# Optimization experiments

Measured on AMD Instinct MI355X. Metric: run time of the kernel, lower is better.

Reference implementation:

```python
import jax, jax.numpy as jnp
import numpy as np

B, T, D, H = 512, 256, 256, 1024


def setup_inputs() -> dict:
    key = jax.random.key(0)
    ks = jax.random.split(key, 8)
    s = 1.0 / np.sqrt(3 * D)
    return {
        "X": jax.random.normal(ks[0], (B, T, D), dtype=jnp.float32),
        "M": (jax.random.uniform(ks[1], (B, T, D)) < 0.5).astype(jnp.float32),
        "input_means": jax.random.normal(ks[2], (D,), dtype=jnp.float32) * 0.1,
        "gamma_x": jnp.ones((D,), dtype=jnp.float32),
        "Wz": jax.random.normal(ks[3], (H, 3 * D), dtype=jnp.float32) * s,
        "bz": jnp.zeros((H,), dtype=jnp.float32),
        "Wr": jax.random.normal(ks[4], (H, 3 * D), dtype=jnp.float32) * s,
        "br": jnp.zeros((H,), dtype=jnp.float32),
        "Wh": jax.random.normal(ks[5], (H, 3 * D), dtype=jnp.float32) * s,
        "bh": jnp.zeros((H,), dtype=jnp.float32),
        "Wout": jax.random.normal(ks[6], (1, H), dtype=jnp.float32) * (1.0 / np.sqrt(H)),
        "bout": jnp.zeros((1,), dtype=jnp.float32),
    }


def reference(X, M, input_means, gamma_x, Wz, bz, Wr, br, Wh, bh, Wout, bout):
    Bc, Tc, Dc = X.shape
    xm = input_means  # [D], broadcast as the per-timestep mean
    xm_b = jnp.broadcast_to(xm, (Bc, Dc))

    def step(h, xt_mt):
        x_t, m_t = xt_mt  # each [B, D]
        x_hat = m_t * x_t + (1.0 - m_t) * xm
        g = jnp.exp(-gamma_x * (1.0 - m_t))  # input decay
        x_tilde = g * x_hat + (1.0 - g) * xm
        inp = jnp.concatenate([x_tilde, xm_b, m_t], axis=1)  # [B, 3D]
        z_t = jax.nn.sigmoid(inp @ Wz.T + bz)
        r_t = jax.nn.sigmoid(inp @ Wr.T + br)  # computed but unused (faithful to source)
        h_til = jnp.tanh(inp @ Wh.T + bh)
        h_new = (1.0 - z_t) * h + z_t * h_til
        return h_new, None

    h0 = jnp.zeros((Bc, Wz.shape[0]), dtype=X.dtype)
    # scan over time: only the final hidden state feeds the output head
    h_last, _ = jax.lax.scan(step, h0, (jnp.swapaxes(X, 0, 1), jnp.swapaxes(M, 0, 1)))
    out = jax.nn.sigmoid(h_last @ Wout.T + bout)  # [B, 1]
    return out.squeeze(1)  # [B]
```

## Files before the change

### kernel.cpp

```cpp
#include <hip/hip_runtime.h>
#include <cstdint>
#include <cstddef>

#define B_  512
#define T_  256
#define D_  256
#define H_  1024
#define K2  512
#define N2  2048
#define TC  32
#define NCHUNK 8

#define OFF_WB    ((size_t)0)
#define OFF_CVEC  ((size_t)2097152)
#define OFF_H     ((size_t)2105344)
#define OFF_PQ    ((size_t)4202496)
#define OFF_INP2  ((size_t)37756928)
#define WS_BIG    ((size_t)171974656)

typedef short   bf16x8 __attribute__((ext_vector_type(8)));
typedef float   f32x4  __attribute__((ext_vector_type(4)));

__device__ __forceinline__ unsigned short f2bf(float f) {
    unsigned int u = __float_as_uint(f);
    u += 0x7fffu + ((u >> 16) & 1u);
    return (unsigned short)(u >> 16);
}
__device__ __forceinline__ float bf2f(unsigned short s) {
    return __uint_as_float(((unsigned int)s) << 16);
}
__device__ __forceinline__ void async16(const void* g, void* l) {
    __builtin_amdgcn_global_load_lds(
        (const __attribute__((address_space(1))) void*)g,
        (__attribute__((address_space(3))) void*)l, 16, 0, 0);
}

__global__ void build_wb(const float* __restrict__ Wz, const float* __restrict__ Wh,
                         const float* __restrict__ xm, unsigned short* __restrict__ Wb) {
    int e = blockIdx.x * 256 + threadIdx.x;
    int r = e >> 9;
    int k = e & 511;
    int m = r >> 1;
    const float* W = (r & 1) ? (Wh + (size_t)m * 768) : (Wz + (size_t)m * 768);
    float v = (k < D_) ? W[k]
                       : (W[2 * D_ + (k - D_)] - W[k - D_] * xm[k - D_]);
    Wb[e] = f2bf(v);
}

__global__ void build_cvec(const float* __restrict__ Wz, const float* __restrict__ bz,
                           const float* __restrict__ Wh, const float* __restrict__ bh,
                           const float* __restrict__ xm, float* __restrict__ cvec) {
    int r = blockIdx.x;
    int m = r >> 1;
    int d = threadIdx.x;
    const float* W = (r & 1) ? (Wh + (size_t)m * 768) : (Wz + (size_t)m * 768);
    float v = (W[d] + W[D_ + d]) * xm[d];
    for (int off = 32; off; off >>= 1) v += __shfl_down(v, off);
    __shared__ float red[4];
    if ((d & 63) == 0) red[d >> 6] = v;
    __syncthreads();
    if (d == 0) {
        float bias = (r & 1) ? bh[m] : bz[m];
        cvec[r] = bias + red[0] + red[1] + red[2] + red[3];
    }
}

__global__ void build_inp2(const float* __restrict__ X, const float* __restrict__ Mm,
                           unsigned short* __restrict__ inp2, int chunk0) {
    int g = blockIdx.x * 256 + threadIdx.x;
    int r = g >> 6;
    int k = (g & 63) * 8;
    int c  = chunk0 + (r >> 14);
    int rl = r & 16383;
    int b  = rl >> 5;
    int tc = rl & 31;
    int t  = c * TC + tc;
    int d  = (k < D_) ? k : (k - D_);
    const float4* mp = (const float4*)(Mm + ((size_t)b * T_ + t) * D_ + d);
    float4 m0 = mp[0], m1 = mp[1];
    unsigned short o[8];
    if (k < D_) {
        const float4* xp = (const float4*)(X + ((size_t)b * T_ + t) * D_ + d);
        float4 x0 = xp[0], x1 = xp[1];
        o[0]=f2bf(m0.x*x0.x); o[1]=f2bf(m0.y*x0.y); o[2]=f2bf(m0.z*x0.z); o[3]=f2bf(m0.w*x0.w);
        o[4]=f2bf(m1.x*x1.x); o[5]=f2bf(m1.y*x1.y); o[6]=f2bf(m1.z*x1.z); o[7]=f2bf(m1.w*x1.w);
    } else {
        o[0]=f2bf(m0.x); o[1]=f2bf(m0.y); o[2]=f2bf(m0.z); o[3]=f2bf(m0.w);
        o[4]=f2bf(m1.x); o[5]=f2bf(m1.y); o[6]=f2bf(m1.z); o[7]=f2bf(m1.w);
    }
    uint4 pk;
    pk.x = (unsigned)o[0] | ((unsigned)o[1] << 16);
    pk.y = (unsigned)o[2] | ((unsigned)o[3] << 16);
    pk.z = (unsigned)o[4] | ((unsigned)o[5] << 16);
    pk.w = (unsigned)o[6] | ((unsigned)o[7] << 16);
    *(uint4*)(inp2 + (size_t)r * K2 + k) = pk;
}

#define EPAD 140
__global__ __launch_bounds__(256) void gemm_scan(
    const unsigned short* __restrict__ A,
    const unsigned short* __restrict__ W,
    const float* __restrict__ cvec,
    float2* __restrict__ PQ,
    int chunk0)
{
    __shared__ __align__(16) unsigned short sm[128 * EPAD];
    const int tid  = threadIdx.x;
    const int lane = tid & 63;
    const int w    = tid >> 6;
    const int tn = blockIdx.x, tmg = blockIdx.y;
    const int wm = w & 1, wn = w >> 1;

    const int seg  = w * 2;
    const int srow = seg * 16 + (lane >> 2);
    const int scol = (lane & 3) * 8;
    const int aoff = seg * 512;
    const unsigned short* aptr = A + (size_t)(tmg * 128 + srow) * K2 + scol;
    const unsigned short* bptr = W + (size_t)(tn * 128 + srow) * K2 + scol;

#define STAGE(nxt, k0)                                              \
    { unsigned short* ad = sm + (nxt) * 4096 + aoff;                \
      unsigned short* bd = sm + 8192 + (nxt) * 4096 + aoff;         \
      async16(aptr + (k0),            ad);                          \
      async16(aptr + 16 * K2 + (k0),  ad + 512);                    \
      async16(bptr + (k0),            bd);                          \
      async16(bptr + 16 * K2 + (k0),  bd + 512); }

    f32x4 acc[4][4] = {};

    STAGE(0, 0);
    __syncthreads();

    for (int t = 0; t < 16; ++t) {
        const int cur = t & 1;
        if (t < 15) STAGE(cur ^ 1, (t + 1) * 32);
        const unsigned short* Ab = sm + cur * 4096;
        const unsigned short* Bb = sm + 8192 + cur * 4096;
        bf16x8 af[4], bv[4];
        #pragma unroll
        for (int i = 0; i < 4; i++)
            af[i] = *(const bf16x8*)&Ab[(wm*64 + i*16 + (lane & 15)) * 32 + (lane >> 4) * 8];
        #pragma unroll
        for (int j = 0; j < 4; j++)
            bv[j] = *(const bf16x8*)&Bb[(wn*64 + j*16 + (lane & 15)) * 32 + (lane >> 4) * 8];
        #pragma unroll
        for (int i = 0; i < 4; i++)
            #pragma unroll
            for (int j = 0; j < 4; j++)
                acc[i][j] = __builtin_amdgcn_mfma_f32_16x16x32_bf16(af[i], bv[j], acc[i][j], 0, 0, 0);
        __syncthreads();
    }
#undef STAGE

    const float p = (float)(lane & 1);
    const float sg = 1.f + p;
    #pragma unroll
    for (int j = 0; j < 4; j++) {
        const int ncol  = tn*128 + wn*64 + j*16 + (lane & 15);
        const int col_l = wn*64 + j*16 + (lane & 15);
        const float cadd = cvec[ncol];
        #pragma unroll
        for (int i = 0; i < 4; i++) {
            const int rbase = wm*64 + i*16 + (lane >> 4) * 4;
            #pragma unroll
            for (int r = 0; r < 4; r++) {
                float v = acc[i][j][r] + cadd;
                float u = __expf(-sg * v);
                float res = sg / (1.f + u) - p;
                sm[(size_t)(rbase + r) * EPAD + col_l] = f2bf(res);
            }
        }
    }
    __syncthreads();

    const int bl = tid >> 6;
    const int np = tid & 63;
    const unsigned int* lds32 = (const unsigned int*)sm;
    float Pp = 1.f, Qq = 0.f;
    #pragma unroll
    for (int tc = 0; tc < 32; ++tc) {
        unsigned int zw = lds32[(size_t)(bl * 32 + tc) * (EPAD / 2) + np];
        float z  = bf2f((unsigned short)(zw & 0xffff));
        float ht = bf2f((unsigned short)(zw >> 16));
        float om = 1.f - z;
        Qq = om * Qq + z * ht;
        Pp = om * Pp;
    }
    const int c   = chunk0 + (tmg >> 7);
    const int bg  = (tmg & 127) * 4 + bl;
    const int npg = tn * 64 + np;
    PQ[((size_t)c * B_ + bg) * H_ + npg] = make_float2(Pp, Qq);
}

__global__ void combine(const float2* __restrict__ PQ, float* __restrict__ hbuf) {
    int v = blockIdx.x * 256 + threadIdx.x;
    int b = v >> 10;
    int n = v & 1023;
    float h = 0.f;
    #pragma unroll
    for (int c = 0; c < NCHUNK; c++) {
        float2 pq = PQ[((size_t)c * B_ + b) * H_ + n];
        h = pq.x * h + pq.y;
    }
    hbuf[(size_t)b * H_ + n] = h;
}

__global__ void head(const float* __restrict__ hbuf, const float* __restrict__ Wout,
                     const float* __restrict__ bout, float* __restrict__ out) {
    int b = blockIdx.x;
    float s = 0.f;
    for (int n = threadIdx.x; n < H_; n += 256)
        s += hbuf[(size_t)b * H_ + n] * Wout[n];
    for (int off = 32; off; off >>= 1) s += __shfl_down(s, off);
    __shared__ float red[4];
    if ((threadIdx.x & 63) == 0) red[threadIdx.x >> 6] = s;
    __syncthreads();
    if (threadIdx.x == 0) {
        float t = red[0] + red[1] + red[2] + red[3] + bout[0];
        out[b] = 1.f / (1.f + expf(-t));
    }
}

extern "C" void kernel_launch(void* const* d_in, const int* in_sizes, int n_in,
                              void* d_out, int out_size, void* d_ws, size_t ws_size,
                              hipStream_t stream) {
    const float* X    = (const float*)d_in[0];
    const float* Mm   = (const float*)d_in[1];
    const float* xm   = (const float*)d_in[2];
    const float* Wz   = (const float*)d_in[4];
    const float* bz   = (const float*)d_in[5];
    const float* Wh   = (const float*)d_in[8];
    const float* bh   = (const float*)d_in[9];
    const float* Wout = (const float*)d_in[10];
    const float* bout = (const float*)d_in[11];
    float* out = (float*)d_out;

    char* ws = (char*)d_ws;
    unsigned short* Wb    = (unsigned short*)(ws + OFF_WB);
    float*          cvec  = (float*)(ws + OFF_CVEC);
    float*          hbuf  = (float*)(ws + OFF_H);
    float2*         PQ    = (float2*)(ws + OFF_PQ);
    unsigned short* inp2  = (unsigned short*)(ws + OFF_INP2);

    build_wb  <<<dim3(N2 * K2 / 256), dim3(256), 0, stream>>>(Wz, Wh, xm, Wb);
    build_cvec<<<dim3(N2),            dim3(256), 0, stream>>>(Wz, bz, Wh, bh, xm, cvec);

    if (ws_size >= WS_BIG) {
        build_inp2<<<dim3(NCHUNK * TC * B_ * 64 / 256), dim3(256), 0, stream>>>(X, Mm, inp2, 0);
        gemm_scan <<<dim3(16, NCHUNK * TC * B_ / 128),  dim3(256), 0, stream>>>(inp2, Wb, cvec, PQ, 0);
    } else {
        for (int c = 0; c < NCHUNK; c++) {
            build_inp2<<<dim3(TC * B_ * 64 / 256), dim3(256), 0, stream>>>(X, Mm, inp2, c);
            gemm_scan <<<dim3(16, TC * B_ / 128),  dim3(256), 0, stream>>>(inp2, Wb, cvec, PQ, c);
        }
    }

    combine<<<dim3(B_ * H_ / 256), dim3(256), 0, stream>>>(PQ, hbuf);
    head   <<<dim3(B_),            dim3(256), 0, stream>>>(hbuf, Wout, bout, out);
}
```

Measured before the change: 714.4 us.

## Fuse input packing into GEMM-scan, keep full A tile in LDS, scan in registers

Drops the separate build_inp2 pass and its bf16 intermediate buffer. Each 512-thread block now converts its 128 rows of X*M and M to bf16 directly into LDS once, then sweeps all 2048 output columns, reading weights straight from global memory (L2) with no LDS staging. The per-chunk scan is done in registers using lane shuffles and an associative combine of (P,Q) pairs, replacing the LDS round-trip of activations. This removes a large global write and read of the packed input, but weight traffic now goes through L2 without sharing across waves, and the larger accumulator arrays increase register pressure.

Result: slower. 1.571 ms (+119.9%).

```diff
diff --git a/kernel.cpp b/kernel.cpp
--- a/kernel.cpp
+++ b/kernel.cpp
@@ -15,8 +15,6 @@
 #define OFF_CVEC  ((size_t)2097152)
 #define OFF_H     ((size_t)2105344)
 #define OFF_PQ    ((size_t)4202496)
-#define OFF_INP2  ((size_t)37756928)
-#define WS_BIG    ((size_t)171974656)
 
 typedef short   bf16x8 __attribute__((ext_vector_type(8)));
 typedef float   f32x4  __attribute__((ext_vector_type(4)));
@@ -25,14 +23,6 @@
     unsigned int u = __float_as_uint(f);
     u += 0x7fffu + ((u >> 16) & 1u);
     return (unsigned short)(u >> 16);
-}
-__device__ __forceinline__ float bf2f(unsigned short s) {
-    return __uint_as_float(((unsigned int)s) << 16);
-}
-__device__ __forceinline__ void async16(const void* g, void* l) {
-    __builtin_amdgcn_global_load_lds(
-        (const __attribute__((address_space(1))) void*)g,
-        (__attribute__((address_space(3))) void*)l, 16, 0, 0);
 }
 
 __global__ void build_wb(const float* __restrict__ Wz, const float* __restrict__ Wh,
@@ -65,131 +55,133 @@
     }
 }
 
-__global__ void build_inp2(const float* __restrict__ X, const float* __restrict__ Mm,
-                           unsigned short* __restrict__ inp2, int chunk0) {
-    int g = blockIdx.x * 256 + threadIdx.x;
-    int r = g >> 6;
-    int k = (g & 63) * 8;
-    int c  = chunk0 + (r >> 14);
-    int rl = r & 16383;
-    int b  = rl >> 5;
-    int tc = rl & 31;
-    int t  = c * TC + tc;
-    int d  = (k < D_) ? k : (k - D_);
-    const float4* mp = (const float4*)(Mm + ((size_t)b * T_ + t) * D_ + d);
-    float4 m0 = mp[0], m1 = mp[1];
-    unsigned short o[8];
-    if (k < D_) {
-        const float4* xp = (const float4*)(X + ((size_t)b * T_ + t) * D_ + d);
-        float4 x0 = xp[0], x1 = xp[1];
-        o[0]=f2bf(m0.x*x0.x); o[1]=f2bf(m0.y*x0.y); o[2]=f2bf(m0.z*x0.z); o[3]=f2bf(m0.w*x0.w);
-        o[4]=f2bf(m1.x*x1.x); o[5]=f2bf(m1.y*x1.y); o[6]=f2bf(m1.z*x1.z); o[7]=f2bf(m1.w*x1.w);
-    } else {
-        o[0]=f2bf(m0.x); o[1]=f2bf(m0.y); o[2]=f2bf(m0.z); o[3]=f2bf(m0.w);
-        o[4]=f2bf(m1.x); o[5]=f2bf(m1.y); o[6]=f2bf(m1.z); o[7]=f2bf(m1.w);
-    }
-    uint4 pk;
-    pk.x = (unsigned)o[0] | ((unsigned)o[1] << 16);
-    pk.y = (unsigned)o[2] | ((unsigned)o[3] << 16);
-    pk.z = (unsigned)o[4] | ((unsigned)o[5] << 16);
-    pk.w = (unsigned)o[6] | ((unsigned)o[7] << 16);
-    *(uint4*)(inp2 + (size_t)r * K2 + k) = pk;
-}
-
-#define EPAD 140
-__global__ __launch_bounds__(256) void gemm_scan(
-    const unsigned short* __restrict__ A,
+#define ASTRIDE 520
+__global__ __launch_bounds__(512, 2) void gemm_scan(
+    const float* __restrict__ X,
+    const float* __restrict__ Mm,
     const unsigned short* __restrict__ W,
     const float* __restrict__ cvec,
-    float2* __restrict__ PQ,
-    int chunk0)
+    float2* __restrict__ PQ)
 {
-    __shared__ __align__(16) unsigned short sm[128 * EPAD];
+    __shared__ __align__(16) unsigned short As[128 * ASTRIDE];
     const int tid  = threadIdx.x;
     const int lane = tid & 63;
     const int w    = tid >> 6;
-    const int tn = blockIdx.x, tmg = blockIdx.y;
-    const int wm = w & 1, wn = w >> 1;
-
-    const int seg  = w * 2;
-    const int srow = seg * 16 + (lane >> 2);
-    const int scol = (lane & 3) * 8;
-    const int aoff = seg * 512;
-    const unsigned short* aptr = A + (size_t)(tmg * 128 + srow) * K2 + scol;
-    const unsigned short* bptr = W + (size_t)(tn * 128 + srow) * K2 + scol;
-
-#define STAGE(nxt, k0)                                              \
-    { unsigned short* ad = sm + (nxt) * 4096 + aoff;                \
-      unsigned short* bd = sm + 8192 + (nxt) * 4096 + aoff;         \
-      async16(aptr + (k0),            ad);                          \
-      async16(aptr + 16 * K2 + (k0),  ad + 512);                    \
-      async16(bptr + (k0),            bd);                          \
-      async16(bptr + 16 * K2 + (k0),  bd + 512); }
-
-    f32x4 acc[4][4] = {};
-
-    STAGE(0, 0);
+    const int p    = blockIdx.x;
+    const int c    = p >> 7;
+    const int bg0  = (p & 127) * 4;
+
+    {
+        const int half = lane >> 5;
+        const int d    = (lane & 31) * 8;
+        #pragma unroll
+        for (int j = 0; j < 16; ++j) {
+            const int row = w + 8 * j;
+            const int b   = bg0 + (row >> 5);
+            const int t   = c * TC + (row & 31);
+            const size_t base = ((size_t)b * T_ + t) * D_ + d;
+            const float4* mp = (const float4*)(Mm + base);
+            float4 m0 = mp[0], m1 = mp[1];
+            float v[8];
+            if (half == 0) {
+                const float4* xp = (const float4*)(X + base);
+                float4 x0 = xp[0], x1 = xp[1];
+                v[0]=m0.x*x0.x; v[1]=m0.y*x0.y; v[2]=m0.z*x0.z; v[3]=m0.w*x0.w;
+                v[4]=m1.x*x1.x; v[5]=m1.y*x1.y; v[6]=m1.z*x1.z; v[7]=m1.w*x1.w;
+            } else {
+                v[0]=m0.x; v[1]=m0.y; v[2]=m0.z; v[3]=m0.w;
+                v[4]=m1.x; v[5]=m1.y; v[6]=m1.z; v[7]=m1.w;
+            }
+            uint4 pk;
+            pk.x = (unsigned)f2bf(v[0]) | ((unsigned)f2bf(v[1]) << 16);
+            pk.y = (unsigned)f2bf(v[2]) | ((unsigned)f2bf(v[3]) << 16);
+            pk.z = (unsigned)f2bf(v[4]) | ((unsigned)f2bf(v[5]) << 16);
+            pk.w = (unsigned)f2bf(v[6]) | ((unsigned)f2bf(v[7]) << 16);
+            *(uint4*)&As[row * ASTRIDE + lane * 8] = pk;
+        }
+    }
     __syncthreads();
 
-    for (int t = 0; t < 16; ++t) {
-        const int cur = t & 1;
-        if (t < 15) STAGE(cur ^ 1, (t + 1) * 32);
-        const unsigned short* Ab = sm + cur * 4096;
-        const unsigned short* Bb = sm + 8192 + cur * 4096;
-        bf16x8 af[4], bv[4];
+    const int l15 = lane & 15;
+    const int q8  = (lane >> 4) * 8;
+    const float par = (float)(lane & 1);
+    const float sg  = 1.f + par;
+
+    for (int ci = 0; ci < 4; ++ci) {
+        const int nbase = w * 256 + ci * 64;
+        const unsigned short* wp0 = W + (size_t)(nbase +  0 + l15) * K2 + q8;
+        const unsigned short* wp1 = wp0 + 16 * K2;
+        const unsigned short* wp2 = wp0 + 32 * K2;
+        const unsigned short* wp3 = wp0 + 48 * K2;
+
+        f32x4 acc[8][4] = {};
         #pragma unroll
-        for (int i = 0; i < 4; i++)
-            af[i] = *(const bf16x8*)&Ab[(wm*64 + i*16 + (lane & 15)) * 32 + (lane >> 4) * 8];
+        for (int kk = 0; kk < 16; ++kk) {
+            bf16x8 af[8], bv[4];
+            #pragma unroll
+            for (int i = 0; i < 8; ++i)
+                af[i] = *(const bf16x8*)&As[(i * 16 + l15) * ASTRIDE + q8 + kk * 32];
+            bv[0] = *(const bf16x8*)(wp0 + kk * 32);
+            bv[1] = *(const bf16x8*)(wp1 + kk * 32);
+            bv[2] = *(const bf16x8*)(wp2 + kk * 32);
+            bv[3] = *(const bf16x8*)(wp3 + kk * 32);
+            #pragma unroll
+            for (int i = 0; i < 8; ++i)
+                #pragma unroll
+                for (int j = 0; j < 4; ++j)
+                    acc[i][j] = __builtin_amdgcn_mfma_f32_16x16x32_bf16(af[i], bv[j], acc[i][j], 0, 0, 0);
+        }
+
         #pragma unroll
-        for (int j = 0; j < 4; j++)
-            bv[j] = *(const bf16x8*)&Bb[(wn*64 + j*16 + (lane & 15)) * 32 + (lane >> 4) * 8];
-        #pragma unroll
-        for (int i = 0; i < 4; i++)
+        for (int j = 0; j < 4; ++j) {
+            const float cadd = cvec[nbase + j * 16 + l15];
             #pragma unroll
-            for (int j = 0; j < 4; j++)
-                acc[i][j] = __builtin_amdgcn_mfma_f32_16x16x32_bf16(af[i], bv[j], acc[i][j], 0, 0, 0);
-        __syncthreads();
-    }
-#undef STAGE
-
-    const float p = (float)(lane & 1);
-    const float sg = 1.f + p;
-    #pragma unroll
-    for (int j = 0; j < 4; j++) {
-        const int ncol  = tn*128 + wn*64 + j*16 + (lane & 15);
-        const int col_l = wn*64 + j*16 + (lane & 15);
-        const float cadd = cvec[ncol];
-        #pragma unroll
-        for (int i = 0; i < 4; i++) {
-            const int rbase = wm*64 + i*16 + (lane >> 4) * 4;
-            #pragma unroll
-            for (int r = 0; r < 4; r++) {
-                float v = acc[i][j][r] + cadd;
-                float u = __expf(-sg * v);
-                float res = sg / (1.f + u) - p;
-                sm[(size_t)(rbase + r) * EPAD + col_l] = f2bf(res);
+            for (int bl = 0; bl < 4; ++bl) {
+                float PA = 1.f, QA = 0.f, PB = 1.f, QB = 0.f;
+                #pragma unroll
+                for (int r = 0; r < 4; ++r) {
+                    {
+                        float v  = acc[2 * bl][j][r] + cadd;
+                        float a  = sg / (1.f + __expf(-sg * v)) - par;
+                        float ap = __shfl_xor(a, 1);
+                        float z  = (lane & 1) ? ap : a;
+                        float ht = (lane & 1) ? a : ap;
+                        float om = 1.f - z;
+                        QA = om * QA + z * ht;
+                        PA = om * PA;
+                    }
+                    {
+                        float v  = acc[2 * bl + 1][j][r] + cadd;
+                        float a  = sg / (1.f + __expf(-sg * v)) - par;
+                        float ap = __shfl_xor(a, 1);
+                        float z  = (lane & 1) ? ap : a;
+                        float ht = (lane & 1) ? a : ap;
+                        float om = 1.f - z;
+                        QB = om * QB + z * ht;
+                        PB = om * PB;
+                    }
+                }
+                #pragma unroll
+                for (int s = 16; s <= 32; s <<= 1) {
+                    float PAp = __shfl_xor(PA, s), QAp = __shfl_xor(QA, s);
+                    float PBp = __shfl_xor(PB, s), QBp = __shfl_xor(QB, s);
+                    const bool late = (lane & s) != 0;
+                    float Pe = late ? PAp : PA,  Qe = late ? QAp : QA;
+                    float Pl = late ? PA  : PAp, Ql = late ? QA  : QAp;
+                    PA = Pl * Pe;  QA = Pl * Qe + Ql;
+                    Pe = late ? PBp : PB;  Qe = late ? QBp : QB;
+                    Pl = late ? PB  : PBp; Ql = late ? QB  : QBp;
+                    PB = Pl * Pe;  QB = Pl * Qe + Ql;
+                }
+                const float Ptot = PB * PA;
+                const float Qtot = PB * QA + QB;
+                if (((lane >> 4) == bl) && ((lane & 1) == 0)) {
+                    const int npg = (nbase + j * 16 + l15) >> 1;
+                    PQ[((size_t)c * B_ + bg0 + bl) * H_ + npg] = make_float2(Ptot, Qtot);
+                }
             }
         }
     }
-    __syncthreads();
-
-    const int bl = tid >> 6;
-    const int np = tid & 63;
-    const unsigned int* lds32 = (const unsigned int*)sm;
-    float Pp = 1.f, Qq = 0.f;
-    #pragma unroll
-    for (int tc = 0; tc < 32; ++tc) {
-        unsigned int zw = lds32[(size_t)(bl * 32 + tc) * (EPAD / 2) + np];
-        float z  = bf2f((unsigned short)(zw & 0xffff));
-        float ht = bf2f((unsigned short)(zw >> 16));
-        float om = 1.f - z;
-        Qq = om * Qq + z * ht;
-        Pp = om * Pp;
-    }
-    const int c   = chunk0 + (tmg >> 7);
-    const int bg  = (tmg & 127) * 4 + bl;
-    const int npg = tn * 64 + np;
-    PQ[((size_t)c * B_ + bg) * H_ + npg] = make_float2(Pp, Qq);
 }
 
 __global__ void combine(const float2* __restrict__ PQ, float* __restrict__ hbuf) {
@@ -240,20 +232,11 @@
     float*          cvec  = (float*)(ws + OFF_CVEC);
     float*          hbuf  = (float*)(ws + OFF_H);
     float2*         PQ    = (float2*)(ws + OFF_PQ);
-    unsigned short* inp2  = (unsigned short*)(ws + OFF_INP2);
 
     build_wb  <<<dim3(N2 * K2 / 256), dim3(256), 0, stream>>>(Wz, Wh, xm, Wb);
     build_cvec<<<dim3(N2),            dim3(256), 0, stream>>>(Wz, bz, Wh, bh, xm, cvec);
 
-    if (ws_size >= WS_BIG) {
-        build_inp2<<<dim3(NCHUNK * TC * B_ * 64 / 256), dim3(256), 0, stream>>>(X, Mm, inp2, 0);
-        gemm_scan <<<dim3(16, NCHUNK * TC * B_ / 128),  dim3(256), 0, stream>>>(inp2, Wb, cvec, PQ, 0);
-    } else {
-        for (int c = 0; c < NCHUNK; c++) {
-            build_inp2<<<dim3(TC * B_ * 64 / 256), dim3(256), 0, stream>>>(X, Mm, inp2, c);
-            gemm_scan <<<dim3(16, TC * B_ / 128),  dim3(256), 0, stream>>>(inp2, Wb, cvec, PQ, c);
-        }
-    }
+    gemm_scan<<<dim3(NCHUNK * TC * B_ / 128), dim3(512), 0, stream>>>(X, Mm, Wb, cvec, PQ);
 
     combine<<<dim3(B_ * H_ / 256), dim3(256), 0, stream>>>(PQ, hbuf);
     head   <<<dim3(B_),            dim3(256), 0, stream>>>(hbuf, Wout, bout, out);
```
